# Optimization experiments

Hardware: AMD Instinct MI355X
Metric: run time of the kernel (lower is better)

The kernel has to match this reference:

```python
import math
import jax, jax.numpy as jnp
import numpy as np

NUM_HEADS = 8
TOP_M = 5
CLAMP_LOGIT = 2.0
LN_EPS = 1e-5


def _layernorm(x, w, b):
    m = jnp.mean(x, axis=-1, keepdims=True)
    v = jnp.mean((x - m) ** 2, axis=-1, keepdims=True)
    return (x - m) * jax.lax.rsqrt(v + LN_EPS) * w + b


def _l2norm(x, eps=1e-6):
    n = jnp.sqrt(jnp.sum(x * x, axis=-1, keepdims=True))
    return x / jnp.maximum(n, eps)


def setup_inputs() -> dict:
    key = jax.random.key(0)
    ks = jax.random.split(key, 20)
    B, H, W, Cv = 8, 64, 64, 512
    T, Ct = 77, 512
    s = 0.02
    inp = {
        'visual_features': jax.random.normal(ks[0], (B, H, W, Cv), jnp.float32),
        'text_features': jax.random.normal(ks[1], (B, T, Ct), jnp.float32),
        'norm1_w': jnp.ones((Cv,), jnp.float32),
        'norm1_b': jnp.zeros((Cv,), jnp.float32),
        'Wq': jax.random.normal(ks[2], (Cv, Cv), jnp.float32) * s,
        'bq': jnp.zeros((Cv,), jnp.float32),
        'Wk': jax.random.normal(ks[3], (Ct, Cv), jnp.float32) * s,
        'bk': jnp.zeros((Cv,), jnp.float32),
        'Wv': jax.random.normal(ks[4], (Ct, Cv), jnp.float32) * s,
        'bv': jnp.zeros((Cv,), jnp.float32),
        'Wo': jax.random.normal(ks[5], (Cv, Cv), jnp.float32) * s,
        'bo': jnp.zeros((Cv,), jnp.float32),
        'gate_w': jax.random.normal(ks[6], (Cv, 1), jnp.float32) * s,
        'gate_b': jnp.zeros((1,), jnp.float32),
        'norm2_w': jnp.ones((Cv,), jnp.float32),
        'norm2_b': jnp.zeros((Cv,), jnp.float32),
        'ffn_w1': jax.random.normal(ks[7], (Cv, 4 * Cv), jnp.float32) * s,
        'ffn_b1': jnp.zeros((4 * Cv,), jnp.float32),
        'ffn_w2': jax.random.normal(ks[8], (4 * Cv, Cv), jnp.float32) * s,
        'ffn_b2': jnp.zeros((Cv,), jnp.float32),
        'logit_scale': jnp.asarray(math.log(1.0 / 0.07), jnp.float32),
        'alpha': jnp.asarray(0.1, jnp.float32),
    }
    return inp


def reference(visual_features, text_features, norm1_w, norm1_b, Wq, bq, Wk, bk,
              Wv, bv, Wo, bo, gate_w, gate_b, norm2_w, norm2_b,
              ffn_w1, ffn_b1, ffn_w2, ffn_b2, logit_scale, alpha):
    B, H, W, Cv = visual_features.shape
    N = H * W
    Hh = NUM_HEADS
    Dh = Cv // Hh

    # Pre-LN + projections
    x = _layernorm(visual_features, norm1_w, norm1_b).reshape(B, N, Cv)
    q_full = x @ Wq + bq                       # (B,N,Cv)
    k_full = text_features @ Wk + bk           # (B,T,Cv)
    v_full = text_features @ Wv + bv           # (B,T,Cv)

    # pad mask: all-zero text tokens (B,T)
    pad_mask = jnp.sum(jnp.abs(text_features), axis=-1) <= 1e-6

    # cosine attention: normalize over full Cv before splitting heads (as in source)
    q = _l2norm(q_full).reshape(B, N, Hh, Dh)
    k = _l2norm(k_full).reshape(B, -1, Hh, Dh)
    v = v_full.reshape(B, -1, Hh, Dh)

    scale = jnp.exp(jnp.clip(logit_scale, -CLAMP_LOGIT, CLAMP_LOGIT)) / math.sqrt(Dh)
    sim = jnp.einsum('bnhd,bthd->bnht', q, k) * scale  # (B,N,Hh,T)
    sim = jnp.where(pad_mask[:, None, None, :], -jnp.inf, sim)

    # top-k sparsification along text dim (keep entries >= k-th largest)
    if TOP_M < sim.shape[-1]:
        topv = jax.lax.top_k(sim, TOP_M)[0]
        kth = topv[..., -1:]
        sim = jnp.where(sim >= kth, sim, -jnp.inf)

    attn = jax.nn.softmax(sim, axis=-1)
    aligned = jnp.einsum('bnht,bthd->bnhd', attn, v).reshape(B, N, Cv)
    aligned = aligned @ Wo + bo

    gate = jax.nn.sigmoid(x @ gate_w + gate_b)  # (B,N,1)
    y = x + alpha * gate * aligned
    y = _layernorm(y, norm2_w, norm2_b)
    h = jax.nn.gelu(y @ ffn_w1 + ffn_b1, approximate=False)
    y = y + (h @ ffn_w2 + ffn_b2)
    return y.reshape(B, H, W, Cv)
```

## Files before the change

kernel.cpp:

```cpp
#include <hip/hip_runtime.h>
#include <hip/hip_bf16.h>
#include <math.h>

constexpr int Bv = 8;
constexpr int Nv = 4096;
constexpr int Cvd = 512;
constexpr int Tt = 77;
constexpr int Dh = 64;
constexpr int MROWS = Bv * Nv;
constexpr int KTROWS = Bv * Tt;

typedef __attribute__((ext_vector_type(8))) short bf16x8;
typedef __attribute__((ext_vector_type(4))) float f32x4;

__device__ __forceinline__ float bfbits2f(short s) {
    unsigned int u = ((unsigned int)(unsigned short)s) << 16;
    return __uint_as_float(u);
}
__device__ __forceinline__ short f2bfbits(float f) {
    __hip_bfloat16 h = __float2bfloat16(f);
    return *reinterpret_cast<short*>(&h);
}

__device__ __forceinline__ void gload16(const void* g, void* l) {
    __builtin_amdgcn_global_load_lds(
        (const __attribute__((address_space(1))) void*)g,
        (__attribute__((address_space(3))) void*)l, 16, 0, 0);
}

__device__ __forceinline__ void block_barrier() {
    asm volatile("" ::: "memory");
    __builtin_amdgcn_s_barrier();
    asm volatile("" ::: "memory");
}

__global__ __launch_bounds__(256)
void wtrans4_kernel(const float* __restrict__ Wq, const float* __restrict__ Wo,
                    const float* __restrict__ w1, const float* __restrict__ w2,
                    __hip_bfloat16* __restrict__ WqT, __hip_bfloat16* __restrict__ WoT,
                    __hip_bfloat16* __restrict__ w1T, __hip_bfloat16* __restrict__ w2T)
{
    __shared__ float tile[32][33];
    const int bid = blockIdx.x;
    const float* in;
    __hip_bfloat16* out;
    int K, N, tid;
    if (bid < 256)       { in = Wq; out = WqT; K = 512;  N = 512;  tid = bid; }
    else if (bid < 512)  { in = Wo; out = WoT; K = 512;  N = 512;  tid = bid - 256; }
    else if (bid < 1536) { in = w1; out = w1T; K = 512;  N = 2048; tid = bid - 512; }
    else                 { in = w2; out = w2T; K = 2048; N = 512;  tid = bid - 1536; }
    const int nx = N >> 5;
    const int n0 = (tid % nx) * 32, k0 = (tid / nx) * 32;
    const int tx = threadIdx.x & 31, ty = threadIdx.x >> 5;
    #pragma unroll
    for (int i = ty; i < 32; i += 8)
        tile[i][tx] = in[(size_t)(k0 + i) * N + n0 + tx];
    __syncthreads();
    #pragma unroll
    for (int i = ty; i < 32; i += 8)
        out[(size_t)(n0 + i) * K + k0 + tx] = __float2bfloat16(tile[tx][i]);
}

template<bool GATE, bool WF32>
__global__ __launch_bounds__(128)
void ln_kernel(const float* __restrict__ in, const float* __restrict__ w,
               const float* __restrict__ b, float* __restrict__ out,
               __hip_bfloat16* __restrict__ out_bf,
               const float* __restrict__ gate_w, const float* __restrict__ gate_b,
               float* __restrict__ gate_out)
{
    __shared__ float red[4];
    __shared__ float redg[2];
    const int row = blockIdx.x;
    const int t = threadIdx.x;
    const int wv = t >> 6;
    const float4 v = ((const float4*)(in + (size_t)row * Cvd))[t];

    float s  = v.x + v.y + v.z + v.w;
    float ss = v.x*v.x + v.y*v.y + v.z*v.z + v.w*v.w;
    #pragma unroll
    for (int o = 1; o < 64; o <<= 1) {
        s  += __shfl_xor(s,  o);
        ss += __shfl_xor(ss, o);
    }
    if ((t & 63) == 0) { red[wv*2] = s; red[wv*2+1] = ss; }
    __syncthreads();
    s  = red[0] + red[2];
    ss = red[1] + red[3];
    const float m   = s * (1.0f / 512.0f);
    const float var = ss * (1.0f / 512.0f) - m * m;
    const float rs  = 1.0f / sqrtf(var + 1e-5f);

    const float4 w4 = ((const float4*)w)[t];
    const float4 b4 = ((const float4*)b)[t];
    float4 o4;
    o4.x = (v.x - m) * rs * w4.x + b4.x;
    o4.y = (v.y - m) * rs * w4.y + b4.y;
    o4.z = (v.z - m) * rs * w4.z + b4.z;
    o4.w = (v.w - m) * rs * w4.w + b4.w;
    if (WF32) ((float4*)(out + (size_t)row * Cvd))[t] = o4;

    __hip_bfloat162 h0, h1;
    h0.x = __float2bfloat16(o4.x); h0.y = __float2bfloat16(o4.y);
    h1.x = __float2bfloat16(o4.z); h1.y = __float2bfloat16(o4.w);
    __hip_bfloat16* obp = out_bf + (size_t)row * Cvd + 4*t;
    *(__hip_bfloat162*)(obp)     = h0;
    *(__hip_bfloat162*)(obp + 2) = h1;

    if (GATE) {
        const float4 g4 = ((const float4*)gate_w)[t];
        float g = o4.x*g4.x + o4.y*g4.y + o4.z*g4.z + o4.w*g4.w;
        #pragma unroll
        for (int o = 1; o < 64; o <<= 1) g += __shfl_xor(g, o);
        if ((t & 63) == 0) redg[wv] = g;
        __syncthreads();
        if (t == 0) {
            const float gt = redg[0] + redg[1] + gate_b[0];
            gate_out[row] = 1.0f / (1.0f + expf(-gt));
        }
    }
}

__global__ __launch_bounds__(64)
void knorm_mask_kernel(const float* __restrict__ kf, const float* __restrict__ text,
                       float* __restrict__ msk, __hip_bfloat16* __restrict__ kbf)
{
    const int row = blockIdx.x;
    const int l = threadIdx.x;
    const float4* rp = (const float4*)(kf + (size_t)row * Cvd);
    const float4* tp = (const float4*)(text + (size_t)row * Cvd);
    const float4 a = rp[l], c = rp[l + 64];
    const float4 ta = tp[l], tc = tp[l + 64];
    float ss = a.x*a.x + a.y*a.y + a.z*a.z + a.w*a.w
             + c.x*c.x + c.y*c.y + c.z*c.z + c.w*c.w;
    float sa = fabsf(ta.x)+fabsf(ta.y)+fabsf(ta.z)+fabsf(ta.w)
             + fabsf(tc.x)+fabsf(tc.y)+fabsf(tc.z)+fabsf(tc.w);
    #pragma unroll
    for (int o = 1; o < 64; o <<= 1) {
        ss += __shfl_xor(ss, o);
        sa += __shfl_xor(sa, o);
    }
    const float ki = 1.0f / fmaxf(sqrtf(ss), 1e-6f);
    if (l == 0) msk[row] = (sa <= 1e-6f) ? 1.0f : 0.0f;

    __hip_bfloat16* kp = kbf + (size_t)row * Cvd;
    __hip_bfloat162 p;
    p.x = __float2bfloat16(a.x * ki); p.y = __float2bfloat16(a.y * ki);
    *(__hip_bfloat162*)(kp + l*4)     = p;
    p.x = __float2bfloat16(a.z * ki); p.y = __float2bfloat16(a.w * ki);
    *(__hip_bfloat162*)(kp + l*4 + 2) = p;
    p.x = __float2bfloat16(c.x * ki); p.y = __float2bfloat16(c.y * ki);
    *(__hip_bfloat162*)(kp + (l+64)*4)     = p;
    p.x = __float2bfloat16(c.z * ki); p.y = __float2bfloat16(c.w * ki);
    *(__hip_bfloat162*)(kp + (l+64)*4 + 2) = p;
}

__global__ __launch_bounds__(256)
void gemm32kv_kernel(const float* __restrict__ A,
                     const float* __restrict__ Wk, const float* __restrict__ bk,
                     float* __restrict__ Ck,
                     const float* __restrict__ Wv, const float* __restrict__ bv,
                     float* __restrict__ Cv2,
                     int M, int K)
{
    __shared__ float As[16][64 + 4];
    __shared__ float Bs[16][64 + 4];

    const float* W    = blockIdx.z ? Wv  : Wk;
    const float* bias = blockIdx.z ? bv  : bk;
    float*       C    = blockIdx.z ? Cv2 : Ck;

    const int t = threadIdx.x;
    const int tx = t & 15, ty = t >> 4;
    const int row0 = blockIdx.y * 64;
    const int col0 = blockIdx.x * 64;

    const int arow = t >> 2;
    const int ak   = (t & 3) << 2;
    const int brow = t >> 4;
    const int bcol = (t & 15) << 2;

    float acc[4][4] = {};

    for (int kt = 0; kt < K; kt += 16) {
        float4 a4 = make_float4(0.f, 0.f, 0.f, 0.f);
        const int gr = row0 + arow;
        if (gr < M) a4 = *(const float4*)(A + (size_t)gr * 512 + kt + ak);
        As[ak + 0][arow] = a4.x;
        As[ak + 1][arow] = a4.y;
        As[ak + 2][arow] = a4.z;
        As[ak + 3][arow] = a4.w;
        const float4 b4 = *(const float4*)(W + (size_t)(kt + brow) * 512 + col0 + bcol);
        *(float4*)&Bs[brow][bcol] = b4;
        __syncthreads();
        #pragma unroll
        for (int k = 0; k < 16; k++) {
            const float4 av = *(const float4*)&As[k][ty << 2];
            const float4 bv4 = *(const float4*)&Bs[k][tx << 2];
            acc[0][0] += av.x * bv4.x; acc[0][1] += av.x * bv4.y;
            acc[0][2] += av.x * bv4.z; acc[0][3] += av.x * bv4.w;
            acc[1][0] += av.y * bv4.x; acc[1][1] += av.y * bv4.y;
            acc[1][2] += av.y * bv4.z; acc[1][3] += av.y * bv4.w;
            acc[2][0] += av.z * bv4.x; acc[2][1] += av.z * bv4.y;
            acc[2][2] += av.z * bv4.z; acc[2][3] += av.z * bv4.w;
            acc[3][0] += av.w * bv4.x; acc[3][1] += av.w * bv4.y;
            acc[3][2] += av.w * bv4.z; acc[3][3] += av.w * bv4.w;
        }
        __syncthreads();
    }

    #pragma unroll
    for (int i = 0; i < 4; i++) {
        const int r = row0 + (ty << 2) + i;
        if (r >= M) continue;
        #pragma unroll
        for (int j = 0; j < 4; j++) {
            const int c = col0 + (tx << 2) + j;
            C[(size_t)r * 512 + c] = acc[i][j] + bias[c];
        }
    }
}

enum { EPI_NONE = 0, EPI_WO = 1, EPI_GELU = 2, EPI_RES = 3, EPI_QBF = 4 };

template<int NT, int EPI>
__global__ __launch_bounds__(256, 3)
void bgemm_kernel(const __hip_bfloat16* __restrict__ Ah,
                  const __hip_bfloat16* __restrict__ Bth,
                  const float* __restrict__ bias,
                  void* __restrict__ Cout,
                  int M, int N,
                  const float* __restrict__ xres,
                  const float* __restrict__ gate,
                  const float* __restrict__ alpha_p,
                  const void* __restrict__ yres)
{
    constexpr int K = NT * 32;
    __shared__ short lds[3 * 8192];

    const short* A  = (const short*)Ah;
    const short* Bt = (const short*)Bth;

    const int nwg = gridDim.x;
    const int cpx = nwg >> 3;
    const int bid0 = blockIdx.x;
    const int bid = (bid0 & 7) * cpx + (bid0 >> 3);
    const int cols = N >> 7;
    const int row0 = (bid / cols) << 7;
    const int col0 = (bid % cols) << 7;

    const int t = threadIdx.x;
    const int w = t >> 6, l = t & 63;
    const int wr = w >> 1, wc = w & 1;

    const int src_kelem = (((l & 3) ^ ((l >> 3) & 3)) << 3);
    const short* pA0;
    const short* pA1;
    const short* pB0;
    const short* pB1;
    {
        const int r0 = (2*w)*16 + (l >> 2);
        const int r1 = (2*w + 1)*16 + (l >> 2);
        pA0 = A  + (size_t)(row0 + r0) * K + src_kelem;
        pA1 = A  + (size_t)(row0 + r1) * K + src_kelem;
        pB0 = Bt + (size_t)(col0 + r0) * K + src_kelem;
        pB1 = Bt + (size_t)(col0 + r1) * K + src_kelem;
    }
    short* const dA = lds + (2*w) * 512;
    short* const dB = lds + 4096 + (2*w) * 512;

    auto STAGE = [&](int kt, int bW) {
        gload16(pA0 + kt * 32, dA + bW * 8192);
        gload16(pA1 + kt * 32, dA + bW * 8192 + 512);
        gload16(pB0 + kt * 32, dB + bW * 8192);
        gload16(pB1 + kt * 32, dB + bW * 8192 + 512);
    };

    const int axk = (((l >> 4) << 4) ^ (((l >> 1) & 3) << 4));
    const char* const bA = (const char*)lds + (wr*64 + (l & 15))*64 + axk;
    const char* const bB = (const char*)lds + 8192 + (wc*64 + (l & 15))*64 + axk;

    bf16x8 a[4], b[4];
    f32x4 acc[4][4] = {};

    auto RD = [&](int bR) {
        #pragma unroll
        for (int i = 0; i < 4; i++)
            a[i] = *(const bf16x8*)(bA + bR*16384 + i*1024);
        #pragma unroll
        for (int i = 0; i < 4; i++)
            b[i] = *(const bf16x8*)(bB + bR*16384 + i*1024);
    };
    auto MF = [&]() {
        __builtin_amdgcn_s_setprio(1);
        #pragma unroll
        for (int i = 0; i < 4; i++)
            #pragma unroll
            for (int ni = 0; ni < 4; ni++)
                acc[i][ni] = __builtin_amdgcn_mfma_f32_16x16x32_bf16(
                    a[i], b[ni], acc[i][ni], 0, 0, 0);
        __builtin_amdgcn_s_setprio(0);
    };

    STAGE(0, 0); STAGE(1, 1);
    asm volatile("s_waitcnt vmcnt(4)" ::: "memory");
    block_barrier();

    #pragma unroll
    for (int kt = 0; kt < NT; ++kt) {
        const int bR = kt % 3;
        RD(bR);
        if (kt + 2 < NT) {
            STAGE(kt + 2, (kt + 2) % 3);
            asm volatile("s_waitcnt vmcnt(4)" ::: "memory");
        } else if (kt + 1 < NT) {
            asm volatile("s_waitcnt vmcnt(0)" ::: "memory");
        }
        block_barrier();
        MF();
        if (kt + 1 < NT) block_barrier();
    }

    if (EPI == EPI_QBF) {
        float* qsum = (float*)Cout == nullptr ? nullptr : (float*)(size_t)0;
        (void)qsum;
        #pragma unroll
        for (int mi = 0; mi < 4; mi++) {
            #pragma unroll
            for (int r = 0; r < 4; r++) {
                const int rr = row0 + wr*64 + mi*16 + ((l >> 4) << 2) + r;
                float ssq = 0.0f;
                #pragma unroll
                for (int ni = 0; ni < 4; ni++) {
                    const int c = col0 + wc*64 + ni*16 + (l & 15);
                    const float val = acc[mi][ni][r] + bias[c];
                    ((__hip_bfloat16*)Cout)[(size_t)rr * N + c] = __float2bfloat16(val);
                    ssq += val * val;
                }
                #pragma unroll
                for (int o = 1; o < 16; o <<= 1) ssq += __shfl_xor(ssq, o);
                if ((l & 15) == 0) atomicAdd((float*)xres + rr, ssq);
            }
        }
        return;
    }

    const float alpha = (EPI == EPI_WO) ? alpha_p[0] : 0.0f;
    #pragma unroll
    for (int mi = 0; mi < 4; mi++) {
        const int rbase = row0 + wr*64 + mi*16 + ((l >> 4) << 2);
        #pragma unroll
        for (int ni = 0; ni < 4; ni++) {
            const int c = col0 + wc*64 + ni*16 + (l & 15);
            const float bc = bias[c];
            #pragma unroll
            for (int r = 0; r < 4; r++) {
                const int rr = rbase + r;
                const size_t idx = (size_t)rr * N + c;
                float val = acc[mi][ni][r] + bc;
                if (EPI == EPI_GELU) {
                    const float u = 1.5957691216f * val
                                  + 0.0713548163f * val * val * val;
                    val = val / (1.0f + __expf(-u));
                    ((__hip_bfloat16*)Cout)[idx] = __float2bfloat16(val);
                } else if (EPI == EPI_WO) {
                    ((float*)Cout)[idx] = xres[idx] + alpha * gate[rr] * val;
                } else if (EPI == EPI_RES) {
                    ((float*)Cout)[idx] = bfbits2f(((const short*)yres)[idx]) + val;
                } else {
                    ((float*)Cout)[idx] = val;
                }
            }
        }
    }
}

__global__ __launch_bounds__(256)
void attn_kernel(const __hip_bfloat16* __restrict__ qf,
                 const __hip_bfloat16* __restrict__ kbf,
                 const float* __restrict__ vf,
                 const float* __restrict__ qsum,
                 const float* __restrict__ msk,
                 const float* __restrict__ logit_scale,
                 __hip_bfloat16* __restrict__ out)
{
    __shared__ short kb[80 * 72];
    __shared__ float v_lds[Tt][68];
    __shared__ float qinv_s[256];
    __shared__ float bias_s[80];

    const int gid = blockIdx.x;
    const int b = gid >> 7;
    const int h = (gid >> 4) & 7;
    const int ntile = gid & 15;
    const int t = threadIdx.x;
    const int row0 = b * Nv + ntile * 256;

    #pragma unroll
    for (int it = 0; it < 3; ++it) {
        const int ch = t + it * 256;
        if (ch < 616) {
            const int row = ch >> 3, part = ch & 7;
            *(bf16x8*)&kb[row * 72 + part * 8] =
                *(const bf16x8*)(kbf + (size_t)(b * Tt + row) * Cvd + h * Dh + part * 8);
        }
    }
    if (t < 27) {
        const bf16x8 z = {0,0,0,0,0,0,0,0};
        *(bf16x8*)&kb[77 * 72 + t * 8] = z;
    }
    for (int idx = t; idx < Tt * Dh; idx += 256) {
        const int tt = idx >> 6, dd = idx & 63;
        v_lds[tt][dd] = vf[(size_t)(b * Tt + tt) * Cvd + h * Dh + dd];
    }
    qinv_s[t] = 1.0f / fmaxf(sqrtf(qsum[row0 + t]), 1e-6f);
    if (t < 80) bias_s[t] = (t < 77 && msk[b * Tt + t] == 0.0f) ? 0.0f : -1e30f;
    __syncthreads();

    float ls = logit_scale[0];
    ls = fminf(fmaxf(ls, -2.0f), 2.0f);
    const float scale = __expf(ls) * 0.125f;

    const int w = t >> 6, l = t & 63;
    const int c = l & 15, g = l >> 4;

    bf16x8 qfrag[8];
    #pragma unroll
    for (int rt = 0; rt < 4; ++rt)
        #pragma unroll
        for (int kk = 0; kk < 2; ++kk)
            qfrag[rt*2 + kk] = *(const bf16x8*)(qf +
                (size_t)(row0 + w*64 + rt*16 + c) * Cvd + h * Dh + kk*32 + g*8);

    #pragma unroll
    for (int rt = 0; rt < 4; ++rt) {
        const int lrow = w*64 + rt*16 + c;
        const float qsc = qinv_s[lrow] * scale;

        float v0=-INFINITY,v1=-INFINITY,v2=-INFINITY,v3=-INFINITY,v4=-INFINITY;
        int   i0=0,i1=0,i2=0,i3=0,i4=0;
        auto INS = [&](float s, int idx) {
            const bool c0=s>v0, c1=s>v1, c2=s>v2, c3=s>v3, c4=s>v4;
            const float nv0=c0?s:v0;              const int ni0=c0?idx:i0;
            const float nv1=c1?(c0?v0:s):v1;      const int ni1=c1?(c0?i0:idx):i1;
            const float nv2=c2?(c1?v1:s):v2;      const int ni2=c2?(c1?i1:idx):i2;
            const float nv3=c3?(c2?v2:s):v3;      const int ni3=c3?(c2?i2:idx):i3;
            const float nv4=c4?(c3?v3:s):v4;      const int ni4=c4?(c3?i3:idx):i4;
            v0=nv0;v1=nv1;v2=nv2;v3=nv3;v4=nv4;
            i0=ni0;i1=ni1;i2=ni2;i3=ni3;i4=ni4;
        };

        #pragma unroll
        for (int kt = 0; kt < 5; ++kt) {
            f32x4 acc = {0.f, 0.f, 0.f, 0.f};
            const bf16x8 ka0 = *(const bf16x8*)&kb[(kt*16 + c) * 72 + g*8];
            const bf16x8 ka1 = *(const bf16x8*)&kb[(kt*16 + c) * 72 + 32 + g*8];
            acc = __builtin_amdgcn_mfma_f32_16x16x32_bf16(ka0, qfrag[rt*2+0], acc, 0, 0, 0);
            acc = __builtin_amdgcn_mfma_f32_16x16x32_bf16(ka1, qfrag[rt*2+1], acc, 0, 0, 0);
            #pragma unroll
            for (int r = 0; r < 4; ++r) {
                const int key = kt*16 + g*4 + r;
                INS(acc[r] * qsc + bias_s[key], key);
            }
        }

        #pragma unroll
        for (int st = 16; st <= 32; st <<= 1) {
            const float m0=__shfl_xor(v0,st), m1=__shfl_xor(v1,st),
                        m2=__shfl_xor(v2,st), m3=__shfl_xor(v3,st),
                        m4=__shfl_xor(v4,st);
            const int   j0=__shfl_xor(i0,st), j1=__shfl_xor(i1,st),
                        j2=__shfl_xor(i2,st), j3=__shfl_xor(i3,st),
                        j4=__shfl_xor(i4,st);
            INS(m0,j0); INS(m1,j1); INS(m2,j2); INS(m3,j3); INS(m4,j4);
        }

        const float e1=__expf(v1-v0), e2=__expf(v2-v0),
                    e3=__expf(v3-v0), e4=__expf(v4-v0);
        const float inv = 1.0f / (1.0f + e1 + e2 + e3 + e4);
        const float w0=inv, w1=e1*inv, w2=e2*inv, w3=e3*inv, w4=e4*inv;

        float o[16];
        #pragma unroll
        for (int d4 = 0; d4 < 4; ++d4) {
            const int dd = g*16 + d4*4;
            const float4 p0 = *(const float4*)&v_lds[i0][dd];
            const float4 p1 = *(const float4*)&v_lds[i1][dd];
            const float4 p2 = *(const float4*)&v_lds[i2][dd];
            const float4 p3 = *(const float4*)&v_lds[i3][dd];
            const float4 p4 = *(const float4*)&v_lds[i4][dd];
            o[d4*4+0] = w0*p0.x + w1*p1.x + w2*p2.x + w3*p3.x + w4*p4.x;
            o[d4*4+1] = w0*p0.y + w1*p1.y + w2*p2.y + w3*p3.y + w4*p4.y;
            o[d4*4+2] = w0*p0.z + w1*p1.z + w2*p2.z + w3*p3.z + w4*p4.z;
            o[d4*4+3] = w0*p0.w + w1*p1.w + w2*p2.w + w3*p3.w + w4*p4.w;
        }
        __hip_bfloat16* op = out + (size_t)(row0 + lrow) * Cvd + h * Dh + g*16;
        bf16x8 s0, s1;
        #pragma unroll
        for (int j = 0; j < 8; ++j) { s0[j] = f2bfbits(o[j]); s1[j] = f2bfbits(o[8+j]); }
        *(bf16x8*)op       = s0;
        *(bf16x8*)(op + 8) = s1;
    }
}

extern "C" void kernel_launch(void* const* d_in, const int* in_sizes, int n_in,
                              void* d_out, int out_size, void* d_ws, size_t ws_size,
                              hipStream_t stream)
{
    const float* visual = (const float*)d_in[0];
    const float* text   = (const float*)d_in[1];
    const float* n1w = (const float*)d_in[2];
    const float* n1b = (const float*)d_in[3];
    const float* Wq  = (const float*)d_in[4];
    const float* bq  = (const float*)d_in[5];
    const float* Wk  = (const float*)d_in[6];
    const float* bk  = (const float*)d_in[7];
    const float* Wv  = (const float*)d_in[8];
    const float* bv  = (const float*)d_in[9];
    const float* Wo  = (const float*)d_in[10];
    const float* bo  = (const float*)d_in[11];
    const float* gw  = (const float*)d_in[12];
    const float* gb  = (const float*)d_in[13];
    const float* n2w = (const float*)d_in[14];
    const float* n2b = (const float*)d_in[15];
    const float* w1  = (const float*)d_in[16];
    const float* b1  = (const float*)d_in[17];
    const float* w2  = (const float*)d_in[18];
    const float* b2  = (const float*)d_in[19];
    const float* lsc = (const float*)d_in[20];
    const float* alp = (const float*)d_in[21];

    float* out = (float*)d_out;
    char*  w8  = (char*)d_ws;

    __hip_bfloat16* qbf    = (__hip_bfloat16*)(w8 + 0);
    float*          ypre   = (float*)(w8 + 67108864);
    __hip_bfloat16* hidden = (__hip_bfloat16*)(w8 + 0);
    __hip_bfloat16* xbf    = (__hip_bfloat16*)(w8 + 134217728);
    float*          kf     = (float*)(w8 + 167772160);
    float*          vf     = (float*)(w8 + 169033728);
    float*          qsum   = (float*)(w8 + 170295296);
    float*          mskp   = (float*)(w8 + 170428832);
    float*          gate   = (float*)(w8 + 170431296);
    __hip_bfloat16* WqT    = (__hip_bfloat16*)(w8 + 170562368);
    __hip_bfloat16* WoT    = (__hip_bfloat16*)(w8 + 171086656);
    __hip_bfloat16* w1T    = (__hip_bfloat16*)(w8 + 171610944);
    __hip_bfloat16* w2T    = (__hip_bfloat16*)(w8 + 173708096);
    __hip_bfloat16* kbfg   = (__hip_bfloat16*)(w8 + 175805248);

    wtrans4_kernel<<<dim3(2560), dim3(256), 0, stream>>>(
        Wq, Wo, w1, w2, WqT, WoT, w1T, w2T);
    hipMemsetAsync(qsum, 0, MROWS * sizeof(float), stream);

    ln_kernel<true, true><<<dim3(MROWS), dim3(128), 0, stream>>>(
        visual, n1w, n1b, out, xbf, gw, gb, gate);

    bgemm_kernel<16, EPI_QBF><<<dim3(1024), dim3(256), 0, stream>>>(
        xbf, WqT, bq, qbf, MROWS, 512, qsum, nullptr, nullptr, nullptr);

    gemm32kv_kernel<<<dim3(8, 10, 2), dim3(256), 0, stream>>>(
        text, Wk, bk, kf, Wv, bv, vf, KTROWS, 512);

    knorm_mask_kernel<<<dim3(KTROWS), dim3(64), 0, stream>>>(kf, text, mskp, kbfg);

    attn_kernel<<<dim3(1024), dim3(256), 0, stream>>>(
        qbf, kbfg, vf, qsum, mskp, lsc, xbf);

    bgemm_kernel<16, EPI_WO><<<dim3(1024), dim3(256), 0, stream>>>(
        xbf, WoT, bo, ypre, MROWS, 512, out, gate, alp, nullptr);

    ln_kernel<false, false><<<dim3(MROWS), dim3(128), 0, stream>>>(
        ypre, n2w, n2b, nullptr, xbf, nullptr, nullptr, nullptr);

    bgemm_kernel<16, EPI_GELU><<<dim3(4096), dim3(256), 0, stream>>>(
        xbf, w1T, b1, hidden, MROWS, 2048, nullptr, nullptr, nullptr, nullptr);

    bgemm_kernel<64, EPI_RES><<<dim3(1024), dim3(256), 0, stream>>>(
        hidden, w2T, b2, out, MROWS, 512, nullptr, nullptr, nullptr, xbf);
}
```

Before: 395.1 us.

## Use 256x128-tile double-buffered GEMM kernel for FFN up-projection

Adds a new bf16 MFMA GEMM kernel with 256x128 output tiles (each wave computes 64x128), double-buffered LDS staging and an XCD-aware block remap, and uses it for the FFN1+GELU GEMM in place of the 128x128 triple-buffered kernel. Larger tiles raise arithmetic intensity per LDS/global load and halve the grid. The cost is higher register pressure from 32 accumulators per lane, with launch bounds requesting 3 waves per SIMD, and shallower pipelining with two buffers instead of three. It also removes a dead leftover line in the Q epilogue.

```diff
diff --git a/kernel.cpp b/kernel.cpp
--- a/kernel.cpp
+++ b/kernel.cpp
@@ -322,8 +322,6 @@
     }
 
     if (EPI == EPI_QBF) {
-        float* qsum = (float*)Cout == nullptr ? nullptr : (float*)(size_t)0;
-        (void)qsum;
         #pragma unroll
         for (int mi = 0; mi < 4; mi++) {
             #pragma unroll
@@ -367,6 +365,121 @@
                     ((float*)Cout)[idx] = xres[idx] + alpha * gate[rr] * val;
                 } else if (EPI == EPI_RES) {
                     ((float*)Cout)[idx] = bfbits2f(((const short*)yres)[idx]) + val;
+                } else {
+                    ((float*)Cout)[idx] = val;
+                }
+            }
+        }
+    }
+}
+
+template<int NT, int EPI>
+__global__ __launch_bounds__(256, 3)
+void bgemm256_kernel(const __hip_bfloat16* __restrict__ Ah,
+                     const __hip_bfloat16* __restrict__ Bth,
+                     const float* __restrict__ bias,
+                     void* __restrict__ Cout,
+                     int M, int N)
+{
+    constexpr int K = NT * 32;
+    __shared__ short lds[2 * 12288];
+
+    const short* A  = (const short*)Ah;
+    const short* Bt = (const short*)Bth;
+
+    const int nwg = gridDim.x;
+    const int cpx = nwg >> 3;
+    const int bid0 = blockIdx.x;
+    const int bid = (bid0 & 7) * cpx + (bid0 >> 3);
+    const int cols = N >> 7;
+    const int row0 = (bid / cols) << 8;
+    const int col0 = (bid % cols) << 7;
+
+    const int t = threadIdx.x;
+    const int w = t >> 6, l = t & 63;
+
+    const int src_kelem = (((l & 3) ^ ((l >> 3) & 3)) << 3);
+    const int srow = w*16 + (l >> 2);
+    const short* pA_[4];
+    const short* pB_[2];
+    #pragma unroll
+    for (int j = 0; j < 4; j++)
+        pA_[j] = A + (size_t)(row0 + j*64 + srow) * K + src_kelem;
+    #pragma unroll
+    for (int j = 0; j < 2; j++)
+        pB_[j] = Bt + (size_t)(col0 + j*64 + srow) * K + src_kelem;
+
+    auto STAGE = [&](int kt, int bW) {
+        const int ro = bW * 12288;
+        #pragma unroll
+        for (int j = 0; j < 4; j++)
+            gload16(pA_[j] + kt * 32, lds + ro + (j*64 + w*16) * 32);
+        #pragma unroll
+        for (int j = 0; j < 2; j++)
+            gload16(pB_[j] + kt * 32, lds + ro + 8192 + (j*64 + w*16) * 32);
+    };
+
+    const int axk = (((l >> 4) << 4) ^ (((l >> 1) & 3) << 4));
+    const char* const bA = (const char*)lds + (w*64 + (l & 15))*64 + axk;
+    const char* const bB = (const char*)(lds + 8192) + ((l & 15))*64 + axk;
+
+    bf16x8 a[4], b[8];
+    f32x4 acc[4][8] = {};
+
+    auto RD = [&](int bR) {
+        #pragma unroll
+        for (int i = 0; i < 4; i++)
+            a[i] = *(const bf16x8*)(bA + bR*24576 + i*1024);
+        #pragma unroll
+        for (int i = 0; i < 8; i++)
+            b[i] = *(const bf16x8*)(bB + bR*24576 + i*1024);
+    };
+    auto MF = [&]() {
+        #pragma unroll
+        for (int i = 0; i < 4; i++)
+            #pragma unroll
+            for (int ni = 0; ni < 8; ni++)
+                acc[i][ni] = __builtin_amdgcn_mfma_f32_16x16x32_bf16(
+                    a[i], b[ni], acc[i][ni], 0, 0, 0);
+    };
+
+    STAGE(0, 0); STAGE(1, 1);
+    asm volatile("s_waitcnt vmcnt(6)" ::: "memory");
+    block_barrier();
+
+    #pragma unroll
+    for (int kt = 0; kt < NT; ++kt) {
+        RD(kt & 1);
+        MF();
+        if (kt + 1 < NT) {
+            block_barrier();
+            if (kt + 2 < NT) {
+                STAGE(kt + 2, kt & 1);
+                asm volatile("s_waitcnt vmcnt(6)" ::: "memory");
+            } else {
+                asm volatile("s_waitcnt vmcnt(0)" ::: "memory");
+            }
+            block_barrier();
+        }
+    }
+
+    #pragma unroll
+    for (int mi = 0; mi < 4; mi++) {
+        const int rbase = row0 + w*64 + mi*16 + ((l >> 4) << 2);
+        #pragma unroll
+        for (int ni = 0; ni < 8; ni++) {
+            const int c = col0 + ni*16 + (l & 15);
+            const float bc = bias[c];
+            #pragma unroll
+            for (int r = 0; r < 4; r++) {
+                const int rr = rbase + r;
+                const size_t idx = (size_t)rr * N + c;
+                float val = acc[mi][ni][r] + bc;
+                if (EPI == EPI_GELU) {
+                    const float u = 1.5957691216f * val
+                                  + 0.0713548163f * val * val * val;
+                    val = val / (1.0f + __expf(-u));
+                    ((__hip_bfloat16*)Cout)[idx] = __float2bfloat16(val);
                 } else {
                     ((float*)Cout)[idx] = val;
                 }
@@ -572,8 +685,8 @@
     ln_kernel<false, false><<<dim3(MROWS), dim3(128), 0, stream>>>(
         ypre, n2w, n2b, nullptr, xbf, nullptr, nullptr, nullptr);
 
-    bgemm_kernel<16, EPI_GELU><<<dim3(4096), dim3(256), 0, stream>>>(
-        xbf, w1T, b1, hidden, MROWS, 2048, nullptr, nullptr, nullptr, nullptr);
+    bgemm256_kernel<16, EPI_GELU><<<dim3(2048), dim3(256), 0, stream>>>(
+        xbf, w1T, b1, hidden, MROWS, 2048);
 
     bgemm_kernel<64, EPI_RES><<<dim3(1024), dim3(256), 0, stream>>>(
         hidden, w2T, b2, out, MROWS, 512, nullptr, nullptr, nullptr, xbf);
```

Result: slower. 562.1 us (+42.3%).
